# Kernel tuning notes

Measured on AMD Instinct MI355X. Metric: run time of the kernel, lower is better.

The kernel has to match this reference:

```python
import jax, jax.numpy as jnp
import numpy as np

V, D, L, H, FF, B, S = 32000, 2048, 4, 16, 8192, 2, 2048
DH = D // H
PRUNE_LAYERS = (1, 2)   # layers with an attached pruning module
KEEP_RATIO = 0.5        # keep_ratio arg of forward_prefill_with_pruning


def _rms(x, w, eps=1e-6):
    return x * w * jax.lax.rsqrt(jnp.mean(x * x, -1, keepdims=True) + eps)


def _rope(x):
    # x: [B,H,s,DH]; position_ids = arange(s), recomputed after every pruning step
    s = x.shape[2]
    half = DH // 2
    inv = 1.0 / (10000.0 ** (jnp.arange(half, dtype=jnp.float32) / half))
    ang = jnp.arange(s, dtype=jnp.float32)[:, None] * inv  # [s, half]
    cos, sin = jnp.cos(ang), jnp.sin(ang)
    x1, x2 = x[..., :half], x[..., half:]
    return jnp.concatenate([x1 * cos - x2 * sin, x1 * sin + x2 * cos], -1)


def _block(h, mask, wq, wk, wv, wo, wg, wu, wd, ln1, ln2):
    b, s, _ = h.shape
    hn = _rms(h, ln1)
    q = _rope((hn @ wq).reshape(b, s, H, DH).transpose(0, 2, 1, 3))
    k = _rope((hn @ wk).reshape(b, s, H, DH).transpose(0, 2, 1, 3))
    v = (hn @ wv).reshape(b, s, H, DH).transpose(0, 2, 1, 3)
    att = jnp.einsum('bhqd,bhkd->bhqk', q, k) / np.float32(np.sqrt(DH))
    allowed = jnp.tril(jnp.ones((s, s), bool)) & (mask[:, None, None, :] > 0)
    att = jnp.where(allowed, att, jnp.float32(-1e9))
    o = jnp.einsum('bhqk,bhkd->bhqd', jax.nn.softmax(att, -1), v)
    h = h + o.transpose(0, 2, 1, 3).reshape(b, s, D) @ wo
    hn = _rms(h, ln2)
    h = h + (jax.nn.silu(hn @ wg) * (hn @ wu)) @ wd
    return h


def _forward(input_ids, attention_mask, embed, wq, wk, wv, wo, wg, wu, wd, ln1, ln2, lnf, lm_head, scorer):
    h = embed[input_ids]        # [B,S,D]
    mask = attention_mask
    for i in range(L):
        if i in PRUNE_LAYERS:
            pi = PRUNE_LAYERS.index(i)
            # pruning module: Linear(D->2); keep score = logits[..., 0]
            sc = jnp.einsum('bsd,cd->bsc', h, scorer[pi])[..., 0]
            kk = max(1, int(h.shape[1] * KEEP_RATIO))      # static under jit
            _, idx = jax.lax.top_k(sc, kk)
            idx = jnp.sort(idx, -1)                        # sorted kept indices
            h = jnp.take_along_axis(h, idx[..., None], axis=1)
            mask = jnp.take_along_axis(mask, idx, axis=1)
        h = _block(h, mask, wq[i], wk[i], wv[i], wo[i], wg[i], wu[i], wd[i], ln1[i], ln2[i])
    return _rms(h, lnf) @ lm_head   # logits [B, S_pruned, V]


def setup_inputs() -> dict:
    key = jax.random.key(0)
    ks = jax.random.split(key, 12)
    g = lambda k, shape: jax.random.normal(k, shape, jnp.float32) * 0.02
    return {
        'input_ids': jax.random.randint(ks[0], (B, S), 0, V, jnp.int32),
        'attention_mask': jnp.ones((B, S), jnp.int32),
        'embed': g(ks[1], (V, D)),
        'wq': g(ks[2], (L, D, D)),
        'wk': g(ks[3], (L, D, D)),
        'wv': g(ks[4], (L, D, D)),
        'wo': g(ks[5], (L, D, D)),
        'wg': g(ks[6], (L, D, FF)),
        'wu': g(ks[7], (L, D, FF)),
        'wd': g(ks[8], (L, FF, D)),
        'ln1': jnp.ones((L, D), jnp.float32),
        'ln2': jnp.ones((L, D), jnp.float32),
        'lnf': jnp.ones((D,), jnp.float32),
        'lm_head': g(ks[9], (D, V)),
        'scorer': g(ks[10], (len(PRUNE_LAYERS), 2, D)),
    }


def reference(input_ids, attention_mask, embed, wq, wk, wv, wo, wg, wu, wd, ln1, ln2, lnf, lm_head, scorer):
    return _forward(input_ids, attention_mask, embed, wq, wk, wv, wo, wg, wu, wd, ln1, ln2, lnf, lm_head, scorer)
```

## Files before the change

### kernel.cpp

```cpp
#include <hip/hip_runtime.h>
#include <math.h>


#define DD 2048
#define HH 16
#define DHH 128
#define FFF 8192
#define BBATCH 2
#define SSEQ 2048
#define VV 32000
#define LLAYERS 4

typedef float4 f4;
typedef __attribute__((ext_vector_type(8))) short short8;
typedef __attribute__((ext_vector_type(4))) float f32x4;
typedef unsigned short u16;

__device__ inline u16 bf16rne(float x) {
    unsigned u = __float_as_uint(x);
    unsigned r = (u + 0x7FFFu + ((u >> 16) & 1u)) >> 16;
    return (u16)r;
}
__device__ inline float bf16tof(u16 h) {
    return __uint_as_float(((unsigned)h) << 16);
}

__device__ __forceinline__ void gload16(const u16* g, u16* l) {
    __builtin_amdgcn_global_load_lds(
        (const __attribute__((address_space(1))) unsigned int*)g,
        (__attribute__((address_space(3))) unsigned int*)l, 16, 0, 0);
}

#define BARRIER() do { asm volatile("" ::: "memory"); \
    __builtin_amdgcn_s_barrier(); asm volatile("" ::: "memory"); } while (0)

__device__ __forceinline__ void xcd_swz(int& bx, int& by) {
    int gx = gridDim.x;
    int nwg = gx * gridDim.y;
    int orig = by * gx + bx;
    int q = nwg >> 3, r = nwg & 7;
    int xcd = orig & 7, loc = orig >> 3;
    int swz = (xcd < r ? xcd * (q + 1) : r * (q + 1) + (xcd - r) * q) + loc;
    bx = swz % gx;
    by = swz / gx;
}

__global__ void k_embed(const int* __restrict__ ids, const float* __restrict__ emb,
                        float* __restrict__ out) {
    int row = blockIdx.x;
    int id  = ids[row];
    const f4* src = (const f4*)(emb + (size_t)id * DD);
    f4*       dst = (f4*)(out + (size_t)row * DD);
    for (int i = threadIdx.x; i < DD / 4; i += blockDim.x) dst[i] = src[i];
}

__global__ void k_copy_int(const int* __restrict__ src, int* __restrict__ dst, int n) {
    int i = blockIdx.x * blockDim.x + threadIdx.x;
    if (i < n) dst[i] = src[i];
}

__global__ void k_addN(float* __restrict__ H, const float* __restrict__ P,
                       long len, int nparts) {
    long i = (long)blockIdx.x * 256 + threadIdx.x;
    if (i >= len / 4) return;
    f4 h = ((f4*)H)[i];
    for (int z = 0; z < nparts; z++) {
        f4 p = ((const f4*)(P + (size_t)z * len))[i];
        h.x += p.x; h.y += p.y; h.z += p.z; h.w += p.w;
    }
    ((f4*)H)[i] = h;
}

__global__ __launch_bounds__(256) void k_rmsnorm_cvt(const float* __restrict__ x,
                                                     const float* __restrict__ w,
                                                     u16* __restrict__ OH,
                                                     u16* __restrict__ OL) {
    int row = blockIdx.x;
    const float* xr = x + (size_t)row * DD;
    float ss = 0.f;
    for (int i = threadIdx.x; i < DD / 4; i += blockDim.x) {
        f4 v = ((const f4*)xr)[i];
        ss += v.x * v.x + v.y * v.y + v.z * v.z + v.w * v.w;
    }
    for (int o = 32; o > 0; o >>= 1) ss += __shfl_down(ss, o);
    __shared__ float red[4];
    int wid = threadIdx.x >> 6, lane = threadIdx.x & 63;
    if (lane == 0) red[wid] = ss;
    __syncthreads();
    float tot = red[0] + red[1] + red[2] + red[3];
    float inv = 1.0f / sqrtf(tot / (float)DD + 1e-6f);
    for (int i = threadIdx.x; i < DD / 4; i += blockDim.x) {
        f4 v = ((const f4*)xr)[i];
        f4 wv = ((const f4*)w)[i];
        float o[4];
        o[0] = v.x * wv.x * inv; o[1] = v.y * wv.y * inv;
        o[2] = v.z * wv.z * inv; o[3] = v.w * wv.w * inv;
        ushort4 hv, lv;
        u16* hp = (u16*)&hv; u16* lp = (u16*)&lv;
#pragma unroll
        for (int j = 0; j < 4; j++) {
            u16 h = bf16rne(o[j]);
            hp[j] = h;
            lp[j] = bf16rne(o[j] - bf16tof(h));
        }
        *(ushort4*)&OH[(size_t)row * DD + i * 4] = hv;
        *(ushort4*)&OL[(size_t)row * DD + i * 4] = lv;
    }
}

__global__ __launch_bounds__(256) void k_cvt_w(const float* __restrict__ W,
                                               u16* __restrict__ WtH,
                                               u16* __restrict__ WtL,
                                               int K, int N, int nc0, int dn0,
                                               int writeLo) {
    __shared__ float T[64][65];
    int tid = threadIdx.x;
    int n0g = nc0 + blockIdx.x * 64;
    int k0  = blockIdx.y * 64;
#pragma unroll
    for (int it = 0; it < 4; it++) {
        int r = it * 16 + (tid >> 4);
        int c4 = (tid & 15) * 4;
        f4 v = *(const f4*)(W + (size_t)(k0 + r) * N + n0g + c4);
        T[r][c4 + 0] = v.x; T[r][c4 + 1] = v.y;
        T[r][c4 + 2] = v.z; T[r][c4 + 3] = v.w;
    }
    __syncthreads();
    int nl = tid >> 2;
    int ks = (tid & 3) * 16;
    u16 hi[16], lo[16];
#pragma unroll
    for (int j = 0; j < 16; j++) {
        float v = T[ks + j][nl];
        u16 h = bf16rne(v);
        hi[j] = h;
        lo[j] = bf16rne(v - bf16tof(h));
    }
    size_t base = (size_t)(dn0 + blockIdx.x * 64 + nl) * K + k0 + ks;
    *(short8*)&WtH[base]     = *(short8*)&hi[0];
    *(short8*)&WtH[base + 8] = *(short8*)&hi[8];
    if (writeLo) {
        *(short8*)&WtL[base]     = *(short8*)&lo[0];
        *(short8*)&WtL[base + 8] = *(short8*)&lo[8];
    }
}

template <int PASSES, int RES, int DUAL>
__global__ __launch_bounds__(256, 2) void k_bgemm(const u16* __restrict__ AH,
                                                  const u16* __restrict__ AL,
                                                  const u16* __restrict__ B1H,
                                                  const u16* __restrict__ B1L,
                                                  const u16* __restrict__ B2H,
                                                  const u16* __restrict__ B2L,
                                                  const float* __restrict__ Rsrc,
                                                  float* __restrict__ C,
                                                  u16* __restrict__ OH,
                                                  u16* __restrict__ OL,
                                                  int M, int ldC, int K) {
    constexpr int NW = DUAL ? 2 : 1;
    __shared__ u16 As[128 * 32];
    __shared__ u16 Bs[NW][128 * 32];
    int tid = threadIdx.x;
    int bx = blockIdx.x, by = blockIdx.y;
    xcd_swz(bx, by);
    int m0 = by * 128, n0 = bx * 128;
    int lane = tid & 63, w = tid >> 6;
    int wm = w >> 1, wn = w & 1;
    int lr = lane & 15, lq = lane >> 4;
    int grow = lane >> 2;
    int gcol = (lane & 3) * 8;

    f32x4 acc[NW][4][4];
#pragma unroll
    for (int u = 0; u < NW; u++)
#pragma unroll
        for (int i = 0; i < 4; i++)
#pragma unroll
            for (int j = 0; j < 4; j++)
#pragma unroll
                for (int r = 0; r < 4; r++) acc[u][i][j][r] = 0.f;

    const int KT = PASSES * K;
    for (int kb = 0; kb < KT; kb += 32) {
        int p  = (PASSES > 1) ? ((kb >= 2 * K) ? 2 : ((kb >= K) ? 1 : 0)) : 0;
        int ks = kb - p * K;
        const u16* Ab = ((p == 2) ? AL  : AH)  + (size_t)(m0 + w * 32) * K + ks;
        const u16* Bb = ((p == 1) ? B1L : B1H) + (size_t)(n0 + w * 32) * K + ks;
        __syncthreads();
        gload16(Ab + (size_t)grow * K + gcol,        &As[w * 1024]);
        gload16(Ab + (size_t)(grow + 16) * K + gcol, &As[w * 1024 + 512]);
        gload16(Bb + (size_t)grow * K + gcol,        &Bs[0][w * 1024]);
        gload16(Bb + (size_t)(grow + 16) * K + gcol, &Bs[0][w * 1024 + 512]);
        if constexpr (DUAL) {
            const u16* B2b = ((p == 1) ? B2L : B2H) + (size_t)(n0 + w * 32) * K + ks;
            gload16(B2b + (size_t)grow * K + gcol,        &Bs[1][w * 1024]);
            gload16(B2b + (size_t)(grow + 16) * K + gcol, &Bs[1][w * 1024 + 512]);
        }
        __syncthreads();
        short8 a[4];
#pragma unroll
        for (int i = 0; i < 4; i++)
            a[i] = *(const short8*)&As[(wm * 64 + i * 16 + lr) * 32 + lq * 8];
#pragma unroll
        for (int u = 0; u < NW; u++) {
#pragma unroll
            for (int j = 0; j < 4; j++) {
                short8 b = *(const short8*)&Bs[u][(wn * 64 + j * 16 + lr) * 32 + lq * 8];
#pragma unroll
                for (int i = 0; i < 4; i++)
                    acc[u][i][j] = __builtin_amdgcn_mfma_f32_16x16x32_bf16(
                        a[i], b, acc[u][i][j], 0, 0, 0);
            }
        }
    }
#pragma unroll
    for (int i = 0; i < 4; i++) {
#pragma unroll
        for (int j = 0; j < 4; j++) {
            int gm = m0 + wm * 64 + i * 16 + lq * 4;
            int gn = n0 + wn * 64 + j * 16 + lr;
#pragma unroll
            for (int r = 0; r < 4; r++) {
                size_t off = (size_t)(gm + r) * ldC + gn;
                if constexpr (DUAL) {
                    float g = acc[0][i][j][r], uu = acc[1][i][j][r];
                    float v = g / (1.0f + expf(-g)) * uu;
                    u16 h = bf16rne(v);
                    OH[off] = h;
                    OL[off] = bf16rne(v - bf16tof(h));
                } else {
                    float v = acc[0][i][j][r];
                    if constexpr (RES) v += Rsrc[off];
                    C[off] = v;
                }
            }
        }
    }
}

template <int MH>
__device__ __forceinline__ void loadA256(const u16* SMb, short8 (&aF)[4][2],
                                         int wm, int lr, int lq) {
    const u16* Ab = SMb + MH * 8192;
#pragma unroll
    for (int i = 0; i < 4; i++)
#pragma unroll
        for (int kk = 0; kk < 2; kk++)
            aF[i][kk] = *(const short8*)&Ab[(wm * 64 + i * 16 + lr) * 64 +
                                            (((kk * 4 + lq) ^ (lr & 7)) * 8)];
}

template <int MH, int NH>
__device__ __forceinline__ void quadB256(const u16* SMb, const short8 (&aF)[4][2],
                                         f32x4 (&acc)[8][4], int wn, int lr, int lq) {
    const u16* Bb = SMb + 16384 + NH * 8192;
    short8 bF[2][2];
#pragma unroll
    for (int j = 0; j < 2; j++)
#pragma unroll
        for (int kk = 0; kk < 2; kk++)
            bF[j][kk] = *(const short8*)&Bb[(wn * 32 + j * 16 + lr) * 64 +
                                            (((kk * 4 + lq) ^ (lr & 7)) * 8)];
    __builtin_amdgcn_s_setprio(1);
#pragma unroll
    for (int kk = 0; kk < 2; kk++)
#pragma unroll
        for (int j = 0; j < 2; j++)
#pragma unroll
            for (int i = 0; i < 4; i++)
                acc[MH * 4 + i][NH * 2 + j] = __builtin_amdgcn_mfma_f32_16x16x32_bf16(
                    aF[i][kk], bF[j][kk], acc[MH * 4 + i][NH * 2 + j], 0, 0, 0);
    __builtin_amdgcn_s_setprio(0);
}

template <int PASSES, int PLANE>
__global__ __launch_bounds__(512, 2) void k_bg256(const u16* __restrict__ AH,
                                                  const u16* __restrict__ AL,
                                                  const u16* __restrict__ BH,
                                                  const u16* __restrict__ BL,
                                                  float* __restrict__ C,
                                                  u16* __restrict__ OH,
                                                  u16* __restrict__ OL,
                                                  int M, int ldC, int K, int ld) {
    __shared__ u16 SM[65536];
    int tid = threadIdx.x;
    int bx = blockIdx.x, by = blockIdx.y;
    xcd_swz(bx, by);
    {
        size_t zo = (size_t)blockIdx.z * K;
        AH += zo; BH += zo;
        if constexpr (PASSES > 1) { AL += zo; BL += zo; }
        if constexpr (!PLANE) C += (size_t)blockIdx.z * ((size_t)M * ldC);
    }
    int m0 = by * 256, n0 = bx * 256;
    int w = tid >> 6, lane = tid & 63;
    int wm = w >> 2, wn = w & 3;
    int lr = lane & 15, lq = lane >> 4;

    f32x4 acc[8][4];
#pragma unroll
    for (int i = 0; i < 8; i++)
#pragma unroll
        for (int j = 0; j < 4; j++)
#pragma unroll
            for (int r = 0; r < 4; r++) acc[i][j][r] = 0.f;

    auto ASRC = [&](int T) -> const u16* {
        int kb = T * 64;
        if (PASSES > 1) {
            if (kb >= 2 * K) return AL + (kb - 2 * K);
            if (kb >= K)     return AH + (kb - K);
        }
        return AH + kb;
    };
    auto BSRC = [&](int T) -> const u16* {
        int kb = T * 64;
        if (PASSES > 1) {
            if (kb >= 2 * K) return BH + (kb - 2 * K);
            if (kb >= K)     return BL + (kb - K);
        }
        return BH + kb;
    };
    int srr = lane >> 3;
    int scc = ((lane & 7) ^ srr) * 8;
    auto STAGE_A = [&](int T, int h, int buf) {
        const u16* s = ASRC(T) + (size_t)(m0 + h * 128 + w * 16 + srr) * ld + scc;
        u16* d = SM + buf * 32768 + h * 8192 + w * 16 * 64;
        gload16(s, d);
        gload16(s + (size_t)8 * ld, d + 8 * 64);
    };
    auto STAGE_B = [&](int T, int h, int buf) {
        const u16* s = BSRC(T) + (size_t)(n0 + h * 128 + w * 16 + srr) * ld + scc;
        u16* d = SM + buf * 32768 + 16384 + h * 8192 + w * 16 * 64;
        gload16(s, d);
        gload16(s + (size_t)8 * ld, d + 8 * 64);
    };

    const int NT = (PASSES * K) >> 6;
    STAGE_A(0, 0, 0); STAGE_B(0, 0, 0);
    STAGE_A(0, 1, 0); STAGE_B(0, 1, 0);
    STAGE_A(1, 0, 1); STAGE_B(1, 0, 1);

    for (int T0 = 0; T0 < NT; T0 += 2) {
        int T1 = T0 + 1, T2 = T0 + 2, T3 = T0 + 3;
        short8 aF[4][2];
        STAGE_A(T1, 1, 1);
        asm volatile("s_waitcnt vmcnt(6)" ::: "memory");
        BARRIER();
        loadA256<0>(SM, aF, wm, lr, lq);
        quadB256<0, 0>(SM, aF, acc, wn, lr, lq);
        BARRIER();
        STAGE_B(T1, 1, 1);
        quadB256<0, 1>(SM, aF, acc, wn, lr, lq);
        BARRIER();
        if (T2 < NT) STAGE_A(T2, 0, 0);
        loadA256<1>(SM, aF, wm, lr, lq);
        quadB256<1, 0>(SM, aF, acc, wn, lr, lq);
        BARRIER();
        if (T2 < NT) STAGE_B(T2, 0, 0);
        quadB256<1, 1>(SM, aF, acc, wn, lr, lq);
        BARRIER();
        if (T2 < NT) {
            STAGE_A(T2, 1, 0);
            asm volatile("s_waitcnt vmcnt(6)" ::: "memory");
        } else {
            asm volatile("s_waitcnt vmcnt(0)" ::: "memory");
        }
        BARRIER();
        loadA256<0>(SM + 32768, aF, wm, lr, lq);
        quadB256<0, 0>(SM + 32768, aF, acc, wn, lr, lq);
        BARRIER();
        if (T2 < NT) STAGE_B(T2, 1, 0);
        quadB256<0, 1>(SM + 32768, aF, acc, wn, lr, lq);
        BARRIER();
        if (T3 < NT) STAGE_A(T3, 0, 1);
        loadA256<1>(SM + 32768, aF, wm, lr, lq);
        quadB256<1, 0>(SM + 32768, aF, acc, wn, lr, lq);
        BARRIER();
        if (T3 < NT) STAGE_B(T3, 0, 1);
        quadB256<1, 1>(SM + 32768, aF, acc, wn, lr, lq);
        BARRIER();
    }

#pragma unroll
    for (int i16 = 0; i16 < 8; i16++) {
#pragma unroll
        for (int jj = 0; jj < 4; jj++) {
            int gm = m0 + (i16 >> 2) * 128 + wm * 64 + (i16 & 3) * 16 + lq * 4;
            int gn = n0 + (jj >> 1) * 128 + wn * 32 + (jj & 1) * 16 + lr;
#pragma unroll
            for (int r = 0; r < 4; r++) {
                size_t off = (size_t)(gm + r) * ldC + gn;
                float v = acc[i16][jj][r];
                if constexpr (PLANE) {
                    u16 h = bf16rne(v);
                    OH[off] = h;
                    OL[off] = bf16rne(v - bf16tof(h));
                } else {
                    C[off] = v;
                }
            }
        }
    }
}

__global__ __launch_bounds__(256) void k_silu_cvt(const u16* __restrict__ Gh,
                                                  const u16* __restrict__ Gl,
                                                  u16* __restrict__ FH,
                                                  u16* __restrict__ FL, long n8) {
    long i = (long)blockIdx.x * 256 + threadIdx.x;
    if (i >= n8) return;
    short8 gh = ((const short8*)Gh)[i], gl = ((const short8*)Gl)[i];
    short8 uh = ((const short8*)FH)[i], ul = ((const short8*)FL)[i];
    short8 oh, ol;
#pragma unroll
    for (int e = 0; e < 8; e++) {
        float g = bf16tof((u16)gh[e]) + bf16tof((u16)gl[e]);
        float u = bf16tof((u16)uh[e]) + bf16tof((u16)ul[e]);
        float v = g / (1.0f + expf(-g)) * u;
        u16 h = bf16rne(v);
        oh[e] = (short)h;
        ol[e] = (short)bf16rne(v - bf16tof(h));
    }
    ((short8*)FH)[i] = oh;
    ((short8*)FL)[i] = ol;
}

__global__ void k_rope_table(float* __restrict__ cosT, float* __restrict__ sinT) {
    int idx = blockIdx.x * blockDim.x + threadIdx.x;
    if (idx >= SSEQ * 64) return;
    int pos = idx >> 6, d = idx & 63;
    float p   = (float)pow(10000.0, (double)d * (1.0 / 64.0));
    float inv = 1.0f / p;
    float ang = (float)pos * inv;
    cosT[idx] = (float)cos((double)ang);
    sinT[idx] = (float)sin((double)ang);
}

__global__ void k_rope(float* __restrict__ C,
                       const float* __restrict__ cosT, const float* __restrict__ sinT,
                       int s, int ld) {
    int bi = blockIdx.x;
    int h = bi % HH;
    int i = (bi / HH) % s;
    size_t base = (size_t)(bi / HH) * ld + h * DHH;
    int d = threadIdx.x;
    float c  = cosT[i * 64 + d];
    float sn = sinT[i * 64 + d];
    float x1 = C[base + d], x2 = C[base + 64 + d];
    C[base + d]      = x1 * c - x2 * sn;
    C[base + 64 + d] = x1 * sn + x2 * c;
    x1 = C[base + 2048 + d]; x2 = C[base + 2048 + 64 + d];
    C[base + 2048 + d]      = x1 * c - x2 * sn;
    C[base + 2048 + 64 + d] = x1 * sn + x2 * c;
}

__global__ __launch_bounds__(256) void k_cvt_qk(const float* __restrict__ C,
                                                u16* __restrict__ QHp, u16* __restrict__ QLp,
                                                u16* __restrict__ KHp, u16* __restrict__ KLp) {
    int row = blockIdx.x;
    int c = threadIdx.x * 8;
#pragma unroll
    for (int sec = 0; sec < 2; sec++) {
        const float* src = C + (size_t)row * 6144 + sec * 2048 + c;
        u16* dh = (sec ? KHp : QHp) + (size_t)row * 2048 + c;
        u16* dl = (sec ? KLp : QLp) + (size_t)row * 2048 + c;
        u16 hbuf[8], lbuf[8];
#pragma unroll
        for (int q = 0; q < 2; q++) {
            f4 v = *(const f4*)(src + q * 4);
            float a[4] = {v.x, v.y, v.z, v.w};
#pragma unroll
            for (int e = 0; e < 4; e++) {
                u16 h = bf16rne(a[e]);
                hbuf[q * 4 + e] = h;
                lbuf[q * 4 + e] = bf16rne(a[e] - bf16tof(h));
            }
        }
        *(short8*)dh = *(short8*)&hbuf[0];
        *(short8*)dl = *(short8*)&lbuf[0];
    }
}

__global__ __launch_bounds__(256) void k_cvt_vt(const float* __restrict__ C,
                                                u16* __restrict__ VtH,
                                                u16* __restrict__ VtL, int s) {
    __shared__ float T[64][132];
    int bh = blockIdx.y;
    int h = bh & 15, b = bh >> 4;
    int kv0 = blockIdx.x * 64;
    int t = threadIdx.x;
#pragma unroll
    for (int it = 0; it < 8; it++) {
        int kv = it * 8 + (t >> 5);
        int c4 = (t & 31) * 4;
        f4 v = *(const f4*)(C + (size_t)((size_t)b * s + kv0 + kv) * 6144 + 4096 + h * 128 + c4);
        T[kv][c4 + 0] = v.x; T[kv][c4 + 1] = v.y;
        T[kv][c4 + 2] = v.z; T[kv][c4 + 3] = v.w;
    }
    __syncthreads();
    int d = t >> 1, seg = t & 1;
    size_t base = ((size_t)bh * 128 + d) * s + kv0 + seg * 32;
#pragma unroll
    for (int g = 0; g < 4; g++) {
        u16 h8[8], l8[8];
#pragma unroll
        for (int e = 0; e < 8; e++) {
            float v = T[seg * 32 + g * 8 + e][d];
            u16 hh = bf16rne(v);
            h8[e] = hh;
            l8[e] = bf16rne(v - bf16tof(hh));
        }
        int gp = (g ^ ((d >> 1) & 3)) * 8;
        *(short8*)&VtH[base + gp] = *(short8*)&h8[0];
        *(short8*)&VtL[base + gp] = *(short8*)&l8[0];
    }
}

template <int PASSES>
__global__ __launch_bounds__(256, 2) void k_attn_mfma(
        const u16* __restrict__ QHp, const u16* __restrict__ QLp,
        const u16* __restrict__ KHp, const u16* __restrict__ KLp,
        const u16* __restrict__ VtH, const u16* __restrict__ VtL,
        const int* __restrict__ mask,
        u16* __restrict__ OH, u16* __restrict__ OL, int s) {
    __shared__ u16 SM[21504];
    u16* KsH = SM;
    u16* KsL = SM + 4096;
    u16* VsH = SM + 8192;
    u16* VsL = SM + 12288;
    int tid = threadIdx.x, lane = tid & 63, w = tid >> 6;
    int lr = lane & 15, lq = lane >> 4;
    int grow = lane >> 2;
    int sgcol = (((lane & 3) ^ ((lane >> 3) & 3))) * 8;
    int gcol  = (lane & 3) * 8;
    int rc = (lq ^ ((lr >> 1) & 3)) * 8;
    int qt = blockIdx.x, bh = blockIdx.y;
    int h = bh & 15, b = bh >> 4;
    int q0 = qt * 64;
    size_t rb = (size_t)b * s;
    const u16* vtH = VtH + (size_t)bh * 128 * s;
    const u16* vtL = VtL + (size_t)bh * 128 * s;
    u16* PHw = SM + 16384 + w * 1280;
    u16* PLw = PHw + 640;
    const float scale = 0.08838834764831845f;

    short8 qh[4], ql[4];
    {
        const u16* qp = QHp + (rb + q0) * 2048 + h * 128 + w * 32;
#pragma unroll
        for (int it = 0; it < 4; it++)
            gload16(qp + (size_t)(it * 16 + grow) * 2048 + sgcol, SM + w * 2048 + it * 512);
        __syncthreads();
#pragma unroll
        for (int ks = 0; ks < 4; ks++)
            qh[ks] = *(const short8*)&SM[ks * 2048 + (w * 16 + lr) * 32 + rc];
        if constexpr (PASSES > 1) {
            __syncthreads();
            const u16* qp2 = QLp + (rb + q0) * 2048 + h * 128 + w * 32;
#pragma unroll
            for (int it = 0; it < 4; it++)
                gload16(qp2 + (size_t)(it * 16 + grow) * 2048 + sgcol, SM + w * 2048 + it * 512);
            __syncthreads();
#pragma unroll
            for (int ks = 0; ks < 4; ks++)
                ql[ks] = *(const short8*)&SM[ks * 2048 + (w * 16 + lr) * 32 + rc];
        }
    }

    f32x4 o_acc[8];
#pragma unroll
    for (int j = 0; j < 8; j++)
#pragma unroll
        for (int r = 0; r < 4; r++) o_acc[j][r] = 0.f;
    float m_run[4], l_run[4];
#pragma unroll
    for (int r = 0; r < 4; r++) { m_run[r] = -3.0e38f; l_run[r] = 0.f; }

    int nt = (q0 + 64) >> 5;
    for (int t = 0; t < nt; t++) {
        __syncthreads();
        {
            const u16* kp = KHp + (rb + t * 32) * 2048 + h * 128 + w * 32;
            gload16(kp + (size_t)grow * 2048 + sgcol,        KsH + w * 1024);
            gload16(kp + (size_t)(16 + grow) * 2048 + sgcol, KsH + w * 1024 + 512);
            const u16* vp = vtH + (size_t)(w * 32) * s + t * 32;
            gload16(vp + (size_t)grow * s + gcol,        VsH + (w * 32) * 32);
            gload16(vp + (size_t)(16 + grow) * s + gcol, VsH + (w * 32 + 16) * 32);
            if constexpr (PASSES > 1) {
                const u16* kp2 = KLp + (rb + t * 32) * 2048 + h * 128 + w * 32;
                gload16(kp2 + (size_t)grow * 2048 + sgcol,        KsL + w * 1024);
                gload16(kp2 + (size_t)(16 + grow) * 2048 + sgcol, KsL + w * 1024 + 512);
                const u16* vp2 = vtL + (size_t)(w * 32) * s + t * 32;
                gload16(vp2 + (size_t)grow * s + gcol,        VsL + (w * 32) * 32);
                gload16(vp2 + (size_t)(16 + grow) * s + gcol, VsL + (w * 32 + 16) * 32);
            }
        }
        __syncthreads();
        f32x4 sa[2];
#pragma unroll
        for (int j = 0; j < 2; j++)
#pragma unroll
            for (int r = 0; r < 4; r++) sa[j][r] = 0.f;
#pragma unroll
        for (int j = 0; j < 2; j++) {
#pragma unroll
            for (int ks = 0; ks < 4; ks++) {
                short8 kb = *(const short8*)&KsH[ks * 1024 + (j * 16 + lr) * 32 + rc];
                sa[j] = __builtin_amdgcn_mfma_f32_16x16x32_bf16(qh[ks], kb, sa[j], 0, 0, 0);
                if constexpr (PASSES > 1) {
                    short8 kl2 = *(const short8*)&KsL[ks * 1024 + (j * 16 + lr) * 32 + rc];
                    sa[j] = __builtin_amdgcn_mfma_f32_16x16x32_bf16(qh[ks], kl2, sa[j], 0, 0, 0);
                    sa[j] = __builtin_amdgcn_mfma_f32_16x16x32_bf16(ql[ks], kb, sa[j], 0, 0, 0);
                }
            }
        }
        int mv0 = mask[rb + t * 32 + lr];
        int mv1 = mask[rb + t * 32 + 16 + lr];
        float sclv[4];
#pragma unroll
        for (int r = 0; r < 4; r++) {
            int ig = q0 + w * 16 + lq * 4 + r;
            float v0 = (t * 32 + lr <= ig && mv0 > 0) ? sa[0][r] * scale : -1.0e9f;
            float v1 = (t * 32 + 16 + lr <= ig && mv1 > 0) ? sa[1][r] * scale : -1.0e9f;
            float mx = fmaxf(v0, v1);
            mx = fmaxf(mx, __shfl_xor(mx, 1));
            mx = fmaxf(mx, __shfl_xor(mx, 2));
            mx = fmaxf(mx, __shfl_xor(mx, 4));
            mx = fmaxf(mx, __shfl_xor(mx, 8));
            float mo = m_run[r];
            float mn = fmaxf(mo, mx);
            float p0 = expf(v0 - mn), p1 = expf(v1 - mn);
            float ps = p0 + p1;
            ps += __shfl_xor(ps, 1);
            ps += __shfl_xor(ps, 2);
            ps += __shfl_xor(ps, 4);
            ps += __shfl_xor(ps, 8);
            sclv[r] = expf(mo - mn);
            m_run[r] = mn;
            l_run[r] = l_run[r] * sclv[r] + ps;
            int prow = lq * 4 + r;
            u16 h0 = bf16rne(p0);
            u16 h1 = bf16rne(p1);
            PHw[prow * 40 + lr] = h0;
            PHw[prow * 40 + 16 + lr] = h1;
            if constexpr (PASSES > 1) {
                PLw[prow * 40 + lr] = bf16rne(p0 - bf16tof(h0));
                PLw[prow * 40 + 16 + lr] = bf16rne(p1 - bf16tof(h1));
            }
        }
#pragma unroll
        for (int j = 0; j < 8; j++)
#pragma unroll
            for (int r = 0; r < 4; r++) o_acc[j][r] *= sclv[r];
        short8 ph = *(const short8*)&PHw[lr * 40 + lq * 8];
        short8 pl;
        if constexpr (PASSES > 1) pl = *(const short8*)&PLw[lr * 40 + lq * 8];
#pragma unroll
        for (int j = 0; j < 8; j++) {
            int vrow = j * 16 + lr;
            short8 vh = *(const short8*)&VsH[vrow * 32 + rc];
            o_acc[j] = __builtin_amdgcn_mfma_f32_16x16x32_bf16(ph, vh, o_acc[j], 0, 0, 0);
            if constexpr (PASSES > 1) {
                short8 vl = *(const short8*)&VsL[vrow * 32 + rc];
                o_acc[j] = __builtin_amdgcn_mfma_f32_16x16x32_bf16(ph, vl, o_acc[j], 0, 0, 0);
                o_acc[j] = __builtin_amdgcn_mfma_f32_16x16x32_bf16(pl, vh, o_acc[j], 0, 0, 0);
            }
        }
    }
#pragma unroll
    for (int r = 0; r < 4; r++) {
        float linv = 1.0f / l_run[r];
        size_t rowoff = (rb + q0 + w * 16 + lq * 4 + r) * 2048 + h * 128 + lr;
#pragma unroll
        for (int j = 0; j < 8; j++) {
            float v = o_acc[j][r] * linv;
            u16 hh = bf16rne(v);
            OH[rowoff + j * 16] = hh;
            OL[rowoff + j * 16] = bf16rne(v - bf16tof(hh));
        }
    }
}

__global__ __launch_bounds__(256, 2) void k_attn_f32(const float* __restrict__ Q,
                                                     const float* __restrict__ K,
                                                     const float* __restrict__ V,
                                                     const int* __restrict__ mask,
                                                     u16* __restrict__ OH,
                                                     u16* __restrict__ OL, int s, int ld) {
    int qt = blockIdx.x, bh = blockIdx.y;
    int h = bh & (HH - 1), b = bh >> 4;
    __shared__ float Qs[64][132];
    __shared__ float Ks[32 * 128];
    __shared__ float Vs[32][132];
    __shared__ float Ps[64][36];
    __shared__ float mrow[64], lrow[64];
    int tid = threadIdx.x;
    int tx = tid & 15, ty = tid >> 4;

#pragma unroll
    for (int p = 0; p < 2; p++) {
        int r = p * 32 + (tid >> 3);
        int kb = (tid & 7) * 4;
        const float* src = Q + (size_t)(b * s + qt * 64 + r) * ld + h * DHH;
#pragma unroll
        for (int q = 0; q < 4; q++)
            *(f4*)&Qs[r][kb + 32 * q] = *(const f4*)(src + kb + 32 * q);
    }
    if (tid < 64) { mrow[tid] = -3.0e38f; lrow[tid] = 0.f; }

    float acc[4][8];
#pragma unroll
    for (int i = 0; i < 4; i++)
#pragma unroll
        for (int c = 0; c < 8; c++) acc[i][c] = 0.f;
    const float scale = 0.08838834764831845f;

    int ktmax = 2 * (qt + 1);
    for (int kt = 0; kt < ktmax; kt++) {
        __syncthreads();
#pragma unroll
        for (int p = 0; p < 4; p++) {
            int c = p * 8 + (tid >> 5);
            int kk = (tid & 31) * 4;
            size_t g = (size_t)(b * s + kt * 32 + c) * ld + h * DHH + kk;
            f4 kv = *(const f4*)(K + g);
            int ch = (kk >> 2) ^ (c >> 1);
            *(f4*)&Ks[c * 128 + ch * 4] = kv;
            *(f4*)&Vs[c][kk] = *(const f4*)(V + g);
        }
        __syncthreads();
        float sv[4][2];
#pragma unroll
        for (int i = 0; i < 4; i++) { sv[i][0] = 0.f; sv[i][1] = 0.f; }
        for (int kk = 0; kk < 128; kk += 4) {
            f4 qv[4];
#pragma unroll
            for (int i = 0; i < 4; i++) qv[i] = *(const f4*)&Qs[ty * 4 + i][kk];
#pragma unroll
            for (int j = 0; j < 2; j++) {
                int c = tx * 2 + j;
                int ch = (kk >> 2) ^ (c >> 1);
                f4 kv = *(const f4*)&Ks[c * 128 + ch * 4];
#pragma unroll
                for (int i = 0; i < 4; i++)
                    sv[i][j] += qv[i].x * kv.x + qv[i].y * kv.y +
                                qv[i].z * kv.z + qv[i].w * kv.w;
            }
        }
        float scl[4];
#pragma unroll
        for (int i = 0; i < 4; i++) {
            int r = ty * 4 + i;
            int igl = qt * 64 + r;
#pragma unroll
            for (int j = 0; j < 2; j++) {
                int jg = kt * 32 + tx * 2 + j;
                bool ok = (jg <= igl) && (mask[b * s + jg] > 0);
                sv[i][j] = ok ? sv[i][j] * scale : -1.0e9f;
            }
            float rmax = fmaxf(sv[i][0], sv[i][1]);
            rmax = fmaxf(rmax, __shfl_xor(rmax, 1));
            rmax = fmaxf(rmax, __shfl_xor(rmax, 2));
            rmax = fmaxf(rmax, __shfl_xor(rmax, 4));
            rmax = fmaxf(rmax, __shfl_xor(rmax, 8));
            float mold = mrow[r];
            float mnew = fmaxf(mold, rmax);
            float p0 = expf(sv[i][0] - mnew);
            float p1 = expf(sv[i][1] - mnew);
            float ps = p0 + p1;
            ps += __shfl_xor(ps, 1);
            ps += __shfl_xor(ps, 2);
            ps += __shfl_xor(ps, 4);
            ps += __shfl_xor(ps, 8);
            scl[i] = expf(mold - mnew);
            if (tx == 0) { mrow[r] = mnew; lrow[r] = lrow[r] * scl[i] + ps; }
            float2 pw; pw.x = p0; pw.y = p1;
            *(float2*)&Ps[r][tx * 2] = pw;
        }
        __syncthreads();
#pragma unroll
        for (int i = 0; i < 4; i++) {
            float sc = scl[i];
#pragma unroll
            for (int c = 0; c < 8; c++) acc[i][c] *= sc;
        }
        for (int jj = 0; jj < 32; jj += 4) {
            f4 pv[4];
#pragma unroll
            for (int i = 0; i < 4; i++) pv[i] = *(const f4*)&Ps[ty * 4 + i][jj];
#pragma unroll
            for (int j2 = 0; j2 < 4; j2++) {
                f4 va = *(const f4*)&Vs[jj + j2][tx * 4];
                f4 vb = *(const f4*)&Vs[jj + j2][64 + tx * 4];
#pragma unroll
                for (int i = 0; i < 4; i++) {
                    float p = (&pv[i].x)[j2];
                    acc[i][0] += p * va.x; acc[i][1] += p * va.y;
                    acc[i][2] += p * va.z; acc[i][3] += p * va.w;
                    acc[i][4] += p * vb.x; acc[i][5] += p * vb.y;
                    acc[i][6] += p * vb.z; acc[i][7] += p * vb.w;
                }
            }
        }
    }
    __syncthreads();
#pragma unroll
    for (int i = 0; i < 4; i++) {
        int r = ty * 4 + i;
        float linv = 1.0f / lrow[r];
        size_t ob = (size_t)(b * s + qt * 64 + r) * DD + h * DHH;
        ushort4 h1, l1, h2, l2;
        u16 *h1p = (u16*)&h1, *l1p = (u16*)&l1, *h2p = (u16*)&h2, *l2p = (u16*)&l2;
#pragma unroll
        for (int c = 0; c < 4; c++) {
            float v = acc[i][c] * linv;
            u16 hh = bf16rne(v);
            h1p[c] = hh; l1p[c] = bf16rne(v - bf16tof(hh));
            float v2 = acc[i][c + 4] * linv;
            u16 hh2 = bf16rne(v2);
            h2p[c] = hh2; l2p[c] = bf16rne(v2 - bf16tof(hh2));
        }
        *(ushort4*)&OH[ob + tx * 4] = h1;
        *(ushort4*)&OL[ob + tx * 4] = l1;
        *(ushort4*)&OH[ob + 64 + tx * 4] = h2;
        *(ushort4*)&OL[ob + 64 + tx * 4] = l2;
    }
}

__global__ __launch_bounds__(256) void k_score(const float* __restrict__ Hb,
                                               const float* __restrict__ srow,
                                               float* __restrict__ sc) {
    int row = blockIdx.x;
    const float* xr = Hb + (size_t)row * DD;
    float ss = 0.f;
    for (int i = threadIdx.x; i < DD / 4; i += blockDim.x) {
        f4 a = ((const f4*)xr)[i];
        f4 w = ((const f4*)srow)[i];
        ss += a.x * w.x + a.y * w.y + a.z * w.z + a.w * w.w;
    }
    for (int o = 32; o > 0; o >>= 1) ss += __shfl_down(ss, o);
    __shared__ float red[4];
    int wid = threadIdx.x >> 6, lane = threadIdx.x & 63;
    if (lane == 0) red[wid] = ss;
    __syncthreads();
    if (threadIdx.x == 0) sc[row] = red[0] + red[1] + red[2] + red[3];
}

__global__ __launch_bounds__(256) void k_rank(const float* __restrict__ sc,
                                              int* __restrict__ flg, int s, int kk) {
    int b = blockIdx.x / s, i = blockIdx.x % s;
    const float* scb = sc + (size_t)b * s;
    float vi = scb[i];
    int cnt = 0;
    for (int j = threadIdx.x; j < s; j += 256) {
        float vj = scb[j];
        if (vj > vi || (vj == vi && j < i)) cnt++;
    }
    for (int o = 32; o > 0; o >>= 1) cnt += __shfl_down(cnt, o);
    __shared__ int red[4];
    int wid = threadIdx.x >> 6, lane = threadIdx.x & 63;
    if (lane == 0) red[wid] = cnt;
    __syncthreads();
    if (threadIdx.x == 0) flg[b * s + i] = ((red[0] + red[1] + red[2] + red[3]) < kk) ? 1 : 0;
}

__global__ void k_compact(const int* __restrict__ flg, int* __restrict__ idx, int s, int kk) {
    int b = blockIdx.x;
    if (threadIdx.x == 0) {
        int p = 0;
        for (int i = 0; i < s; i++)
            if (flg[b * s + i]) idx[b * kk + (p++)] = i;
    }
}

__global__ void k_gather(const float* __restrict__ Hin, const int* __restrict__ idx,
                         float* __restrict__ Hout, int s, int kk) {
    int row = blockIdx.x;
    int b = row / kk, p = row % kk;
    int i = idx[b * kk + p];
    const f4* src = (const f4*)(Hin + (size_t)(b * s + i) * DD);
    f4* dst = (f4*)(Hout + (size_t)row * DD);
    for (int t = threadIdx.x; t < DD / 4; t += blockDim.x) dst[t] = src[t];
}

__global__ void k_gather_mask(const int* __restrict__ Min, const int* __restrict__ idx,
                              int* __restrict__ Mout, int s, int kk) {
    int t = blockIdx.x * blockDim.x + threadIdx.x;
    if (t < BBATCH * kk) {
        int b = t / kk, p = t % kk;
        Mout[t] = Min[b * s + idx[b * kk + p]];
    }
}

extern "C" void kernel_launch(void* const* d_in, const int* in_sizes, int n_in,
                              void* d_out, int out_size, void* d_ws, size_t ws_size,
                              hipStream_t stream) {
    const int*   input_ids = (const int*)d_in[0];
    const int*   attn_mask = (const int*)d_in[1];
    const float* embed     = (const float*)d_in[2];
    const float* wq        = (const float*)d_in[3];
    const float* wk        = (const float*)d_in[4];
    const float* wv        = (const float*)d_in[5];
    const float* wo        = (const float*)d_in[6];
    const float* wg        = (const float*)d_in[7];
    const float* wu        = (const float*)d_in[8];
    const float* wd        = (const float*)d_in[9];
    const float* ln1       = (const float*)d_in[10];
    const float* ln2       = (const float*)d_in[11];
    const float* lnf       = (const float*)d_in[12];
    const float* lm_head   = (const float*)d_in[13];
    const float* scorer    = (const float*)d_in[14];

    float* ws = (float*)d_ws;
    const size_t R = (size_t)BBATCH * SSEQ * DD;
    const size_t MISC_FLOATS = 2 * SSEQ * 64 + 5 * (size_t)BBATCH * SSEQ + 1024;
    const size_t NEED_A = (14 * R + MISC_FLOATS) * 4;
    const bool bigws = (ws_size >= NEED_A);

    float* H0   = ws;
    float* H1   = ws + R;
    float* CQKV = ws + 2 * R;
    u16*   AH   = (u16*)(ws + 5 * R);
    u16*   AL   = AH + (size_t)4096 * DD;

    u16* QHp = (u16*)(ws + 6 * R);
    u16* QLp = QHp + (size_t)4096 * DD;
    u16* KHp = (u16*)(ws + 7 * R);
    u16* KLp = KHp + (size_t)4096 * DD;
    u16* VtH = (u16*)(ws + 8 * R);
    u16* VtL = VtH + (size_t)4096 * DD;
    u16* FH  = (u16*)(ws + 6 * R);
    u16* FL  = (u16*)(ws + 8 * R);
    u16* WH1 = (u16*)(ws + 10 * R);
    u16* WL1 = WH1 + (size_t)FFF * DD;
    u16* WH2 = (u16*)(ws + 12 * R);
    u16* WL2 = WH2 + (size_t)FFF * DD;
    u16* WDH = (u16*)(ws + 10 * R);
    u16* WDL = WDH + (size_t)DD * FFF;
    u16* WQKVH = (u16*)(ws + 10 * R);
    u16* WQKVL = WQKVH + (size_t)6144 * DD;

    u16* cWgH = (u16*)CQKV;
    u16* cWgL = cWgH + (size_t)2048 * DD;
    u16* cWuH = cWgL + (size_t)2048 * DD;
    u16* cWuL = cWuH + (size_t)2048 * DD;
    u16* cFH  = (u16*)(ws + 3 * R);
    u16* cFL  = cFH + (size_t)4096 * 2048;
    u16* cWdH = (u16*)(ws + 4 * R);
    u16* cWdL = cWdH + (size_t)2048 * DD;

    float* miscB = ws + (bigws ? 14 * R : 6 * R);
    float* COS = miscB;
    float* SIN = COS + SSEQ * 64;
    float* SC  = SIN + SSEQ * 64;
    int*   FLG = (int*)(SC + (size_t)BBATCH * SSEQ);
    int*   IDX = FLG + BBATCH * SSEQ;
    int*   M0  = IDX + BBATCH * SSEQ;
    int*   M1  = M0 + BBATCH * SSEQ;

    k_rope_table<<<(SSEQ * 64 + 255) / 256, 256, 0, stream>>>(COS, SIN);
    k_embed<<<BBATCH * SSEQ, 256, 0, stream>>>(input_ids, embed, H0);
    k_copy_int<<<(BBATCH * SSEQ + 255) / 256, 256, 0, stream>>>(attn_mask, M0, BBATCH * SSEQ);

    float* Hc = H0; float* Nc = H1;
    int*   Mc = M0; int*   Mt = M1;
    int s = SSEQ;

    for (int l = 0; l < LLAYERS; l++) {
        if (l == 1 || l == 2) {
            int pi = l - 1;
            int kk = s / 2;
            k_score<<<BBATCH * s, 256, 0, stream>>>(Hc, scorer + (size_t)pi * 2 * DD, SC);
            k_rank<<<BBATCH * s, 256, 0, stream>>>(SC, FLG, s, kk);
            k_compact<<<BBATCH, 64, 0, stream>>>(FLG, IDX, s, kk);
            k_gather<<<BBATCH * kk, 256, 0, stream>>>(Hc, IDX, Nc, s, kk);
            k_gather_mask<<<(BBATCH * kk + 255) / 256, 256, 0, stream>>>(Mc, IDX, Mt, s, kk);
            { float* t = Hc; Hc = Nc; Nc = t; }
            { int* t = Mc; Mc = Mt; Mt = t; }
            s = kk;
        }
        int rows = BBATCH * s;
        const bool hiP = (l < 2);
        const int wlo = hiP ? 1 : 0;
        const float* Wq = wq + (size_t)l * DD * DD;
        const float* Wk = wk + (size_t)l * DD * DD;
        const float* Wv = wv + (size_t)l * DD * DD;
        const float* Wo = wo + (size_t)l * DD * DD;
        const float* Wg = wg + (size_t)l * DD * FFF;
        const float* Wu = wu + (size_t)l * DD * FFF;
        const float* Wd = wd + (size_t)l * FFF * DD;
        const float* L1 = ln1 + (size_t)l * DD;
        const float* L2 = ln2 + (size_t)l * DD;

        dim3 gWd(DD / 64, DD / 64);

        k_rmsnorm_cvt<<<rows, 256, 0, stream>>>(Hc, L1, AH, AL);
        if (bigws) {
            k_cvt_w<<<gWd, 256, 0, stream>>>(Wq, WQKVH, WQKVL, DD, DD, 0, 0, wlo);
            k_cvt_w<<<gWd, 256, 0, stream>>>(Wk, WQKVH, WQKVL, DD, DD, 0, 2048, wlo);
            k_cvt_w<<<gWd, 256, 0, stream>>>(Wv, WQKVH, WQKVL, DD, DD, 0, 4096, wlo);
            if (rows >= 2048) {
                dim3 gQKV(6144 / 256, rows / 256);
                if (hiP) k_bg256<3,0><<<gQKV,512,0,stream>>>(AH,AL,WQKVH,WQKVL,CQKV,nullptr,nullptr,rows,6144,DD,DD);
                else     k_bg256<1,0><<<gQKV,512,0,stream>>>(AH,AL,WQKVH,WQKVL,CQKV,nullptr,nullptr,rows,6144,DD,DD);
            } else {
                dim3 gQKV(6144 / 128, rows / 128);
                k_bgemm<1,0,0><<<gQKV,256,0,stream>>>(AH,AL,WQKVH,WQKVL,nullptr,nullptr,nullptr,CQKV,nullptr,nullptr,rows,6144,DD);
            }
        } else {
            u16* WtH = (u16*)Nc;
            u16* WtL = WtH + (size_t)DD * DD;
            dim3 gG(DD / 128, rows / 128);
            const float* Wqkv[3] = {Wq, Wk, Wv};
            for (int q3 = 0; q3 < 3; q3++) {
                k_cvt_w<<<gWd, 256, 0, stream>>>(Wqkv[q3], WtH, WtL, DD, DD, 0, 0, wlo);
                float* Cb = CQKV + q3 * 2048;
                if (hiP) k_bgemm<3,0,0><<<gG,256,0,stream>>>(AH,AL,WtH,WtL,nullptr,nullptr,nullptr,Cb,nullptr,nullptr,rows,6144,DD);
                else     k_bgemm<1,0,0><<<gG,256,0,stream>>>(AH,AL,WtH,WtL,nullptr,nullptr,nullptr,Cb,nullptr,nullptr,rows,6144,DD);
            }
        }
        k_rope<<<rows * HH, 64, 0, stream>>>(CQKV, COS, SIN, s, 6144);

        if (bigws) {
            k_cvt_qk<<<rows, 256, 0, stream>>>(CQKV, QHp, QLp, KHp, KLp);
            k_cvt_vt<<<dim3(s / 64, BBATCH * HH), 256, 0, stream>>>(CQKV, VtH, VtL, s);
            if (hiP) k_attn_mfma<3><<<dim3(s / 64, BBATCH * HH), 256, 0, stream>>>(
                         QHp, QLp, KHp, KLp, VtH, VtL, Mc, AH, AL, s);
            else     k_attn_mfma<1><<<dim3(s / 64, BBATCH * HH), 256, 0, stream>>>(
                         QHp, QLp, KHp, KLp, VtH, VtL, Mc, AH, AL, s);
        } else {
            k_attn_f32<<<dim3(s / 64, BBATCH * HH), 256, 0, stream>>>(
                CQKV, CQKV + 2048, CQKV + 4096, Mc, AH, AL, s, 6144);
        }

        {
            u16* WtH = bigws ? WQKVH : (u16*)Nc;
            u16* WtL = bigws ? (WQKVH + (size_t)DD * DD) : ((u16*)Nc + (size_t)DD * DD);
            k_cvt_w<<<gWd, 256, 0, stream>>>(Wo, WtH, WtL, DD, DD, 0, 0, wlo);
            if (bigws && hiP) {
                int SK = (rows >= 4096) ? 2 : 4;
                float* P = ws + 2 * R;
                dim3 g(DD / 256, rows / 256, SK);
                k_bg256<3,0><<<g, 512, 0, stream>>>(AH, AL, WtH, WtL, P,
                                                    nullptr, nullptr, rows, DD, DD / SK, DD);
                long len = (long)rows * DD;
                k_addN<<<(len / 4 + 255) / 256, 256, 0, stream>>>(Hc, P, len, SK);
            } else {
                dim3 gG(DD / 128, rows / 128);
                if (hiP) k_bgemm<3,1,0><<<gG,256,0,stream>>>(AH,AL,WtH,WtL,nullptr,nullptr,Hc,Hc,nullptr,nullptr,rows,DD,DD);
                else     k_bgemm<1,1,0><<<gG,256,0,stream>>>(AH,AL,WtH,WtL,nullptr,nullptr,Hc,Hc,nullptr,nullptr,rows,DD,DD);
            }
        }

        k_rmsnorm_cvt<<<rows, 256, 0, stream>>>(Hc, L2, AH, AL);
        if (bigws && rows >= 2048) {
            k_cvt_w<<<dim3(FFF / 64, DD / 64), 256, 0, stream>>>(Wg, WH1, WL1, DD, FFF, 0, 0, wlo);
            k_cvt_w<<<dim3(FFF / 64, DD / 64), 256, 0, stream>>>(Wu, WH2, WL2, DD, FFF, 0, 0, wlo);
            u16* Gh = (l == 0) ? (u16*)(ws + R) : (u16*)(ws + 2 * R);
            u16* Gl = (u16*)(ws + 3 * R);
            dim3 gMLP(FFF / 256, rows / 256);
            if (hiP) {
                k_bg256<3,1><<<gMLP,512,0,stream>>>(AH,AL,WH1,WL1,nullptr,Gh,Gl,rows,FFF,DD,DD);
                k_bg256<3,1><<<gMLP,512,0,stream>>>(AH,AL,WH2,WL2,nullptr,FH,FL,rows,FFF,DD,DD);
            } else {
                k_bg256<1,1><<<gMLP,512,0,stream>>>(AH,AL,WH1,WL1,nullptr,Gh,Gl,rows,FFF,DD,DD);
                k_bg256<1,1><<<gMLP,512,0,stream>>>(AH,AL,WH2,WL2,nullptr,FH,FL,rows,FFF,DD,DD);
            }
            long n8 = (long)rows * FFF / 8;
            k_silu_cvt<<<(n8 + 255) / 256, 256, 0, stream>>>(Gh, Gl, FH, FL, n8);
            k_cvt_w<<<dim3(DD / 64, FFF / 64), 256, 0, stream>>>(Wd, WDH, WDL, FFF, DD, 0, 0, wlo);
            int SK = (rows >= 4096) ? 2 : 4;
            float* P = ws + 2 * R;
            dim3 gD(DD / 256, rows / 256, SK);
            if (hiP) k_bg256<3,0><<<gD,512,0,stream>>>(FH,FL,WDH,WDL,P,nullptr,nullptr,rows,DD,FFF/SK,FFF);
            else     k_bg256<1,0><<<gD,512,0,stream>>>(FH,FL,WDH,WDL,P,nullptr,nullptr,rows,DD,FFF/SK,FFF);
            long len = (long)rows * DD;
            k_addN<<<(len / 4 + 255) / 256, 256, 0, stream>>>(Hc, P, len, SK);
        } else if (bigws) {
            k_cvt_w<<<dim3(FFF / 64, DD / 64), 256, 0, stream>>>(Wg, WH1, WL1, DD, FFF, 0, 0, wlo);
            k_cvt_w<<<dim3(FFF / 64, DD / 64), 256, 0, stream>>>(Wu, WH2, WL2, DD, FFF, 0, 0, wlo);
            k_bgemm<1,0,1><<<dim3(FFF/128, rows/128),256,0,stream>>>(AH,AL,WH1,WL1,WH2,WL2,nullptr,nullptr,FH,FL,rows,FFF,DD);
            k_cvt_w<<<dim3(DD / 64, FFF / 64), 256, 0, stream>>>(Wd, WDH, WDL, FFF, DD, 0, 0, wlo);
            k_bgemm<1,1,0><<<dim3(DD/128, rows/128),256,0,stream>>>(FH,FL,WDH,WDL,nullptr,nullptr,Hc,Hc,nullptr,nullptr,rows,DD,FFF);
        } else {
            for (int ffc = 0; ffc < FFF; ffc += 2048) {
                k_cvt_w<<<dim3(2048 / 64, DD / 64), 256, 0, stream>>>(Wg, cWgH, cWgL, DD, FFF, ffc, 0, wlo);
                k_cvt_w<<<dim3(2048 / 64, DD / 64), 256, 0, stream>>>(Wu, cWuH, cWuL, DD, FFF, ffc, 0, wlo);
                if (hiP) k_bgemm<3,0,1><<<dim3(16, rows/128),256,0,stream>>>(AH,AL,cWgH,cWgL,cWuH,cWuL,nullptr,nullptr,cFH,cFL,rows,2048,DD);
                else     k_bgemm<1,0,1><<<dim3(16, rows/128),256,0,stream>>>(AH,AL,cWgH,cWgL,cWuH,cWuL,nullptr,nullptr,cFH,cFL,rows,2048,DD);
                k_cvt_w<<<dim3(DD / 64, 2048 / 64), 256, 0, stream>>>(Wd + (size_t)ffc * DD, cWdH, cWdL, 2048, DD, 0, 0, wlo);
                if (hiP) k_bgemm<3,1,0><<<dim3(DD/128, rows/128),256,0,stream>>>(cFH,cFL,cWdH,cWdL,nullptr,nullptr,Hc,Hc,nullptr,nullptr,rows,DD,2048);
                else     k_bgemm<1,1,0><<<dim3(DD/128, rows/128),256,0,stream>>>(cFH,cFL,cWdH,cWdL,nullptr,nullptr,Hc,Hc,nullptr,nullptr,rows,DD,2048);
            }
        }
    }

    int rows = BBATCH * s;
    u16* AHf = (u16*)Nc;
    u16* ALf = AHf + (size_t)rows * DD;
    u16* LmH = bigws ? (u16*)(ws + 6 * R) : (u16*)CQKV;
    k_rmsnorm_cvt<<<rows, 256, 0, stream>>>(Hc, lnf, AHf, ALf);
    k_cvt_w<<<dim3(VV / 64, DD / 64), 256, 0, stream>>>(lm_head, LmH, LmH, DD, VV, 0, 0, 0);
    if (bigws) {
        k_bg256<1, 0><<<dim3(VV / 256, rows / 256), 512, 0, stream>>>(
            AHf, ALf, LmH, LmH, (float*)d_out, nullptr, nullptr, rows, VV, DD, DD);
    } else {
        k_bgemm<1,0,0><<<dim3(VV / 128, rows / 128), 256, 0, stream>>>(
            AHf, ALf, LmH, LmH, nullptr, nullptr, nullptr, (float*)d_out,
            nullptr, nullptr, rows, VV, DD);
    }
}
```

Baseline: 4.767 ms.

## Double-buffer K/V tiles in MFMA attention and reverse query-tile order

Adds a two-stage LDS ping-pong buffer so the next K/V tile's global-to-LDS loads are issued before computing on the current tile, with explicit vmcnt waits and barriers. Mask loads are prefetched one tile ahead. Query tiles are launched in reverse order so the longest causal tiles start first, which should balance the tail. LDS use roughly doubles, which may reduce occupancy, and the hand-counted vmcnt values assume a fixed number of outstanding loads.

```diff
diff --git a/kernel.cpp b/kernel.cpp
--- a/kernel.cpp
+++ b/kernel.cpp
@@ -524,24 +524,23 @@
         const u16* __restrict__ VtH, const u16* __restrict__ VtL,
         const int* __restrict__ mask,
         u16* __restrict__ OH, u16* __restrict__ OL, int s) {
-    __shared__ u16 SM[21504];
-    u16* KsH = SM;
-    u16* KsL = SM + 4096;
-    u16* VsH = SM + 8192;
-    u16* VsL = SM + 12288;
+    constexpr int BUFU = (PASSES > 1) ? 16384 : 8192;
+    constexpr int VOFF = (PASSES > 1) ? 8192 : 4096;
+    __shared__ u16 SM[2 * BUFU + 5120];
     int tid = threadIdx.x, lane = tid & 63, w = tid >> 6;
     int lr = lane & 15, lq = lane >> 4;
     int grow = lane >> 2;
     int sgcol = (((lane & 3) ^ ((lane >> 3) & 3))) * 8;
     int gcol  = (lane & 3) * 8;
     int rc = (lq ^ ((lr >> 1) & 3)) * 8;
-    int qt = blockIdx.x, bh = blockIdx.y;
+    int qt = gridDim.x - 1 - blockIdx.x;
+    int bh = blockIdx.y;
     int h = bh & 15, b = bh >> 4;
     int q0 = qt * 64;
     size_t rb = (size_t)b * s;
     const u16* vtH = VtH + (size_t)bh * 128 * s;
     const u16* vtL = VtL + (size_t)bh * 128 * s;
-    u16* PHw = SM + 16384 + w * 1280;
+    u16* PHw = SM + 2 * BUFU + w * 1280;
     u16* PLw = PHw + 640;
     const float scale = 0.08838834764831845f;
 
@@ -566,7 +565,26 @@
             for (int ks = 0; ks < 4; ks++)
                 ql[ks] = *(const short8*)&SM[ks * 2048 + (w * 16 + lr) * 32 + rc];
         }
-    }
+        __syncthreads();
+    }
+
+    auto kv_stage = [&](int t, int buf) {
+        u16* base = SM + buf * BUFU;
+        const u16* kp = KHp + (rb + t * 32) * 2048 + h * 128 + w * 32;
+        gload16(kp + (size_t)grow * 2048 + sgcol,        base + w * 1024);
+        gload16(kp + (size_t)(16 + grow) * 2048 + sgcol, base + w * 1024 + 512);
+        const u16* vp = vtH + (size_t)(w * 32) * s + t * 32;
+        gload16(vp + (size_t)grow * s + gcol,        base + VOFF + (w * 32) * 32);
+        gload16(vp + (size_t)(16 + grow) * s + gcol, base + VOFF + (w * 32 + 16) * 32);
+        if constexpr (PASSES > 1) {
+            const u16* kp2 = KLp + (rb + t * 32) * 2048 + h * 128 + w * 32;
+            gload16(kp2 + (size_t)grow * 2048 + sgcol,        base + 4096 + w * 1024);
+            gload16(kp2 + (size_t)(16 + grow) * 2048 + sgcol, base + 4096 + w * 1024 + 512);
+            const u16* vp2 = vtL + (size_t)(w * 32) * s + t * 32;
+            gload16(vp2 + (size_t)grow * s + gcol,        base + 12288 + (w * 32) * 32);
+            gload16(vp2 + (size_t)(16 + grow) * s + gcol, base + 12288 + (w * 32 + 16) * 32);
+        }
+    };
 
     f32x4 o_acc[8];
 #pragma unroll
@@ -578,25 +596,30 @@
     for (int r = 0; r < 4; r++) { m_run[r] = -3.0e38f; l_run[r] = 0.f; }
 
     int nt = (q0 + 64) >> 5;
+    int mv0 = mask[rb + lr];
+    int mv1 = mask[rb + 16 + lr];
+    kv_stage(0, 0);
     for (int t = 0; t < nt; t++) {
-        __syncthreads();
-        {
-            const u16* kp = KHp + (rb + t * 32) * 2048 + h * 128 + w * 32;
-            gload16(kp + (size_t)grow * 2048 + sgcol,        KsH + w * 1024);
-            gload16(kp + (size_t)(16 + grow) * 2048 + sgcol, KsH + w * 1024 + 512);
-            const u16* vp = vtH + (size_t)(w * 32) * s + t * 32;
-            gload16(vp + (size_t)grow * s + gcol,        VsH + (w * 32) * 32);
-            gload16(vp + (size_t)(16 + grow) * s + gcol, VsH + (w * 32 + 16) * 32);
-            if constexpr (PASSES > 1) {
-                const u16* kp2 = KLp + (rb + t * 32) * 2048 + h * 128 + w * 32;
-                gload16(kp2 + (size_t)grow * 2048 + sgcol,        KsL + w * 1024);
-                gload16(kp2 + (size_t)(16 + grow) * 2048 + sgcol, KsL + w * 1024 + 512);
-                const u16* vp2 = vtL + (size_t)(w * 32) * s + t * 32;
-                gload16(vp2 + (size_t)grow * s + gcol,        VsL + (w * 32) * 32);
-                gload16(vp2 + (size_t)(16 + grow) * s + gcol, VsL + (w * 32 + 16) * 32);
-            }
-        }
-        __syncthreads();
+        int bsel = t & 1;
+        if (t + 1 < nt) {
+            kv_stage(t + 1, 1 - bsel);
+            if constexpr (PASSES > 1)
+                asm volatile("s_waitcnt vmcnt(8)" ::: "memory");
+            else
+                asm volatile("s_waitcnt vmcnt(4)" ::: "memory");
+        } else {
+            asm volatile("s_waitcnt vmcnt(0)" ::: "memory");
+        }
+        BARRIER();
+        int nmv0 = mv0, nmv1 = mv1;
+        if (t + 1 < nt) {
+            nmv0 = mask[rb + (t + 1) * 32 + lr];
+            nmv1 = mask[rb + (t + 1) * 32 + 16 + lr];
+        }
+        const u16* KsH = SM + bsel * BUFU;
+        const u16* KsL = KsH + 4096;
+        const u16* VsH = SM + bsel * BUFU + VOFF;
+        const u16* VsL = SM + bsel * BUFU + 12288;
         f32x4 sa[2];
 #pragma unroll
         for (int j = 0; j < 2; j++)
@@ -615,8 +638,6 @@
                 }
             }
         }
-        int mv0 = mask[rb + t * 32 + lr];
-        int mv1 = mask[rb + t * 32 + 16 + lr];
         float sclv[4];
 #pragma unroll
         for (int r = 0; r < 4; r++) {
@@ -667,6 +688,8 @@
                 o_acc[j] = __builtin_amdgcn_mfma_f32_16x16x32_bf16(pl, vh, o_acc[j], 0, 0, 0);
             }
         }
+        BARRIER();
+        mv0 = nmv0; mv1 = nmv1;
     }
 #pragma unroll
     for (int r = 0; r < 4; r++) {
```

Result: no change. 4.740 ms (-0.6%).
